# Kernel optimization log

Measured on AMD Instinct MI355X. Metric: run time of the kernel, lower is better.

The kernel has to match this reference:

```python
import jax, jax.numpy as jnp
import numpy as np

B, S, D, H, O = 256, 512, 256, 256, 128  # batch==hidden per the module's zeros(H,H) init


def setup_inputs() -> dict:
    key = jax.random.key(0)
    ks = jax.random.split(key, 20)
    sc = 0.05
    inp = {
        "x": jax.random.normal(ks[0], (B, S, D), jnp.float32),
        "Wgx_w": jax.random.normal(ks[1], (H, D), jnp.float32) * sc,
        "Wgx_b": jax.random.normal(ks[2], (H,), jnp.float32) * sc,
        "Wgh_w": jax.random.normal(ks[3], (H, H), jnp.float32) * sc,
        "Wgh_b": jax.random.normal(ks[4], (H,), jnp.float32) * sc,
        "Wix_w": jax.random.normal(ks[5], (H, D), jnp.float32) * sc,
        "Wix_b": jax.random.normal(ks[6], (H,), jnp.float32) * sc,
        "Wih_w": jax.random.normal(ks[7], (H, H), jnp.float32) * sc,
        "Wih_b": jax.random.normal(ks[8], (H,), jnp.float32) * sc,
        "Wfx_w": jax.random.normal(ks[9], (H, D), jnp.float32) * sc,
        "Wfx_b": jax.random.normal(ks[10], (H,), jnp.float32) * sc,
        "Wfh_w": jax.random.normal(ks[11], (H, H), jnp.float32) * sc,
        "Wfh_b": jax.random.normal(ks[12], (H,), jnp.float32) * sc,
        "Wox_w": jax.random.normal(ks[13], (H, D), jnp.float32) * sc,
        "Wox_b": jax.random.normal(ks[14], (H,), jnp.float32) * sc,
        "Woh_w": jax.random.normal(ks[15], (H, H), jnp.float32) * sc,
        "Woh_b": jax.random.normal(ks[16], (H,), jnp.float32) * sc,
        "Wph_w": jax.random.normal(ks[17], (O, H), jnp.float32) * sc,
        "Wph_b": jax.random.normal(ks[18], (O,), jnp.float32) * sc,
        "bg": jnp.zeros((B, H), jnp.float32),
        "bi": jnp.zeros((B, H), jnp.float32),
        "bf": jnp.zeros((B, H), jnp.float32),
        "bo": jnp.zeros((B, H), jnp.float32),
        "bp": jnp.zeros((B, O), jnp.float32),
    }
    return inp


def _lstm_forward(x, Wgx_w, Wgx_b, Wgh_w, Wgh_b, Wix_w, Wix_b, Wih_w, Wih_b,
                  Wfx_w, Wfx_b, Wfh_w, Wfh_b, Wox_w, Wox_b, Woh_w, Woh_b,
                  Wph_w, Wph_b, bg, bi, bf, bo, bp):
    b, s, d = x.shape
    h0 = jnp.zeros((b, Wgh_w.shape[0]), x.dtype)  # zeros(H,H) in source; B==H
    c0 = jnp.zeros_like(h0)
    # Precompute the input-to-gate projections for all timesteps (batched GEMM).
    xg = jnp.einsum('bsd,hd->sbh', x, Wgx_w) + Wgx_b + bg  # [S,B,H]
    xi = jnp.einsum('bsd,hd->sbh', x, Wix_w) + Wix_b + bi
    xf = jnp.einsum('bsd,hd->sbh', x, Wfx_w) + Wfx_b + bf
    xo = jnp.einsum('bsd,hd->sbh', x, Wox_w) + Wox_b + bo

    def step(carry, xs):
        h, c = carry
        xg_t, xi_t, xf_t, xo_t = xs
        g = jnp.tanh(xg_t + h @ Wgh_w.T + Wgh_b)
        i = jax.nn.sigmoid(xi_t + h @ Wih_w.T + Wih_b)
        f = jax.nn.sigmoid(xf_t + h @ Wfh_w.T + Wfh_b)
        o = jax.nn.sigmoid(xo_t + h @ Woh_w.T + Woh_b)
        c = g * i + c * f
        h = jnp.tanh(c) * o
        return (h, c), None

    (h, _), _ = jax.lax.scan(step, (h0, c0), (xg, xi, xf, xo))
    p = h @ Wph_w.T + Wph_b + bp
    return jax.nn.softmax(p, axis=1)


def reference(x, Wgx_w, Wgx_b, Wgh_w, Wgh_b, Wix_w, Wix_b, Wih_w, Wih_b,
              Wfx_w, Wfx_b, Wfh_w, Wfh_b, Wox_w, Wox_b, Woh_w, Woh_b,
              Wph_w, Wph_b, bg, bi, bf, bo, bp):
    return _lstm_forward(x, Wgx_w, Wgx_b, Wgh_w, Wgh_b, Wix_w, Wix_b, Wih_w, Wih_b,
                         Wfx_w, Wfx_b, Wfh_w, Wfh_b, Wox_w, Wox_b, Woh_w, Woh_b,
                         Wph_w, Wph_b, bg, bi, bf, bo, bp)
```

## Files before the change

kernel.cpp:

```cpp
#include <hip/hip_runtime.h>
#include <hip/hip_bf16.h>
#include <stdint.h>


typedef unsigned short u16;
typedef unsigned int   u32;
typedef __bf16  bf16x8 __attribute__((ext_vector_type(8)));
typedef float   f32x4  __attribute__((ext_vector_type(4)));

union U4 { uint4 u; bf16x8 b; u16 s[8]; };
union U2 { uint2 u; u16 s[4]; };

static __device__ __forceinline__ u16 f2b(float f){
  union { __hip_bfloat16 h; u16 u; } cv; cv.h = __float2bfloat16(f); return cv.u;
}
static __device__ __forceinline__ float b2f(u16 v){
  union { __hip_bfloat16 h; u16 u; } cv; cv.u = v; return __bfloat162float(cv.h);
}
static __device__ __forceinline__ float fsig(float x){
  return __builtin_amdgcn_rcpf(1.0f + __expf(-x));
}
static __device__ __forceinline__ float ftanh(float x){
  float ax = fabsf(x);
  float t  = __expf(-2.0f*ax);
  float r  = (1.0f - t) * __builtin_amdgcn_rcpf(1.0f + t);
  return copysignf(r, x);
}

struct PrepArgs {
  const float* wx[4]; const float* wh[4];
  const float* wxb[4]; const float* whb[4];
};

__global__ void k_prep(PrepArgs P, u16* __restrict__ WxP, u16* __restrict__ WhP,
                       float* __restrict__ biasj)
{
  int sIdx = blockIdx.x*256 + threadIdx.x;
  int lane = sIdx & 63, kb = (sIdx>>6)&7, jb = sIdx>>9;
  int jp = jb*16 + (lane & 15);
  int gate = jp & 3, hc = jp >> 2;
  int kbase = kb*32 + ((lane>>4)<<3);
  const float* wx = P.wx[gate];
  const float* wh = P.wh[gate];
  U4 ox, oh;
  #pragma unroll
  for (int e=0; e<8; e++){
    ox.s[e] = f2b(wx[hc*256 + kbase + e]);
    oh.s[e] = f2b(wh[hc*256 + kbase + e]);
  }
  *(uint4*)(WxP + (size_t)sIdx*8) = ox.u;
  *(uint4*)(WhP + (size_t)sIdx*8) = oh.u;
  if (sIdx < 1024){
    int g2 = sIdx & 3, h2 = sIdx >> 2;
    biasj[sIdx] = P.wxb[g2][h2] + P.whb[g2][h2];
  }
}

__global__ void k_convx(const float* __restrict__ x, u16* __restrict__ xbf)
{
  int tid = blockIdx.x*256 + threadIdx.x;
  int ch = tid & 31;
  int b  = (tid>>5) & 255;
  int s  = tid >> 13;
  const float* src = x + ((size_t)b*512 + s)*256 + ch*8;
  float4 f0 = *(const float4*)(src);
  float4 f1 = *(const float4*)(src + 4);
  U4 o;
  o.s[0]=f2b(f0.x); o.s[1]=f2b(f0.y); o.s[2]=f2b(f0.z); o.s[3]=f2b(f0.w);
  o.s[4]=f2b(f1.x); o.s[5]=f2b(f1.y); o.s[6]=f2b(f1.z); o.s[7]=f2b(f1.w);
  u32 byteoff = (u32)(s*256 + b)*512u + (((u32)ch*16u) ^ ((u32)(b&7)<<4));
  *(uint4*)((char*)xbf + byteoff) = o.u;
}

__launch_bounds__(512)
__global__ void k_gemm_x(const u16* __restrict__ xbf, const u16* __restrict__ WxP,
                         const float* __restrict__ biasj,
                         const float* __restrict__ bgg, const float* __restrict__ bii,
                         const float* __restrict__ bff, const float* __restrict__ boo,
                         u16* __restrict__ xcat)
{
  __shared__ u16 smA[128*256];
  int tid = threadIdx.x;
  int bid = blockIdx.x;
  int mt = bid >> 2, jt = bid & 3;
  int s = mt >> 1, b0 = (mt & 1)*128;

  const uint4* srcA = (const uint4*)(xbf + (size_t)(s*256 + b0)*256);
  uint4* dstA = (uint4*)smA;
  #pragma unroll
  for (int i=0; i<8; i++) dstA[tid + i*512] = srcA[tid + i*512];
  __syncthreads();

  int lane = tid & 63, wid = tid >> 6;
  int wm = wid >> 2, wn = wid & 3;
  int r16 = lane & 15, khi = lane >> 4;

  f32x4 acc[4][4] = {};
  #pragma unroll
  for (int kb=0; kb<8; kb++){
    bf16x8 a[4];
    #pragma unroll
    for (int mb=0; mb<4; mb++){
      int row = wm*64 + mb*16 + r16;
      u32 abyte = (u32)row*512u + ((u32)((kb*32 + khi*8)*2) ^ ((u32)(row&7)<<4));
      U4 t; t.u = *(const uint4*)((const char*)smA + abyte);
      a[mb] = t.b;
    }
    #pragma unroll
    for (int nb=0; nb<4; nb++){
      int jbg = jt*16 + wn*4 + nb;
      U4 t; t.u = *(const uint4*)(WxP + (size_t)((jbg*8 + kb)*64 + lane)*8);
      #pragma unroll
      for (int mb=0; mb<4; mb++)
        acc[mb][nb] = __builtin_amdgcn_mfma_f32_16x16x32_bf16(a[mb], t.b, acc[mb][nb], 0,0,0);
    }
  }

  int gate = r16 & 3;
  const float* bb = (gate==0) ? bgg : (gate==1) ? bii : (gate==2) ? bff : boo;
  #pragma unroll
  for (int nb=0; nb<4; nb++){
    int jp = jt*256 + wn*64 + nb*16 + r16;
    int hc = jp >> 2;
    float bj = biasj[jp];
    int w_l = wn*2 + (nb>>1);
    int sub = nb & 1;
    #pragma unroll
    for (int mb=0; mb<4; mb++){
      int grp = (b0>>4) + wm*4 + mb;
      U2 pk;
      #pragma unroll
      for (int r=0; r<4; r++){
        int b = b0 + wm*64 + mb*16 + khi*4 + r;
        pk.s[r] = f2b(acc[mb][nb][r] + bj + bb[b*256 + hc]);
      }
      size_t idx = (((size_t)s*16 + grp)*4 + jt)*4096
                 + (size_t)(w_l*64 + khi*16 + r16)*8 + sub*4;
      *(uint2*)(xcat + idx) = pk.u;
    }
  }
}

__launch_bounds__(512, 2)
__global__ void k_lstm(const u16* __restrict__ xcat2, const u16* __restrict__ WhP,
                       u16* __restrict__ hx, int* __restrict__ cnt,
                       float* __restrict__ hfin)
{
  __shared__ u16 hA[2][4096];
  int tid = threadIdx.x, lane = tid & 63, w = tid >> 6;
  int bid = blockIdx.x;
  int xcd = bid & 7, slot = bid >> 3;
  int grp = xcd*2 + (slot>>2), cb = slot & 3;
  int r16 = lane & 15, khi = lane >> 4;
  int gate = r16 & 3, hcl = r16 >> 2;

  bf16x8 wreg[2][8];
  #pragma unroll
  for (int nb=0; nb<2; nb++){
    int jb16 = cb*16 + w*2 + nb;
    #pragma unroll
    for (int kb=0; kb<8; kb++){
      U4 t; t.u = *(const uint4*)(WhP + (size_t)((jb16*8 + kb)*64 + lane)*8);
      wreg[nb][kb] = t.b;
    }
  }

  for (int i=tid; i<4096; i+=512) hA[0][i] = 0;
  __syncthreads();

  const u16* xbase = xcat2 + ((size_t)grp*4 + cb)*4096 + (size_t)tid*8;
  U4 xr; xr.u = *(const uint4*)(xbase);

  float c[2][4] = {};

  for (int t=0; t<512; t++){
    int par = t & 1;
    int tn = (t < 511) ? t+1 : 511;
    U4 xn; xn.u = *(const uint4*)(xbase + (size_t)tn*262144);

    f32x4 acc[2] = {};
    #pragma unroll
    for (int kb=0; kb<8; kb++){
      u32 ab = (u32)r16*512u + (((u32)(kb*64 + khi*16)) ^ ((u32)(r16&7)<<4));
      U4 ta; ta.u = *(const uint4*)((const char*)hA[par] + ab);
      acc[0] = __builtin_amdgcn_mfma_f32_16x16x32_bf16(ta.b, wreg[0][kb], acc[0], 0,0,0);
      acc[1] = __builtin_amdgcn_mfma_f32_16x16x32_bf16(ta.b, wreg[1][kb], acc[1], 0,0,0);
    }

    u16* hxN = hx + (size_t)(((t+1)&1)*16 + grp)*4096;

    #pragma unroll
    for (int nb=0; nb<2; nb++){
      int hc = cb*64 + w*8 + nb*4 + hcl;
      #pragma unroll
      for (int r=0; r<4; r++){
        float v = acc[nb][r] + b2f(xr.s[nb*4+r]);
        float a = (gate==0) ? ftanh(v) : fsig(v);
        float gi = a * __shfl_xor(a, 1);
        float fv = __shfl_xor(a, 2);
        float ov = __shfl_xor(a, 3);
        float cn = gi + c[nb][r]*fv;
        c[nb][r] = cn;
        float hv = ftanh(cn)*ov;
        if (gate == 0){
          u16 hb16 = f2b(hv);
          int b = khi*4 + r;
          hxN[b*256 + hc] = hb16;
          *(u16*)((char*)hA[par^1] +
                  ((u32)b*512u + (((u32)hc*2u) ^ ((u32)(b&7)<<4)))) = hb16;
          if (t == 511) hfin[(grp*16 + b)*256 + hc] = hv;
        }
      }
    }

    __syncthreads();
    if (tid == 0){
      int* cc = cnt + grp*2 + ((t+1)&1);
      __hip_atomic_fetch_add(cc, 1, __ATOMIC_RELEASE, __HIP_MEMORY_SCOPE_AGENT);
      int tgt = 4*((t>>1) + 1);
      while (__hip_atomic_load(cc, __ATOMIC_ACQUIRE, __HIP_MEMORY_SCOPE_AGENT) < tgt)
        __builtin_amdgcn_s_sleep(1);
    }
    __syncthreads();
    if (tid < 384){
      int oc = tid >> 7, rem = tid & 127;
      int b = rem >> 3, hc8 = rem & 7;
      int cbo = (cb + 1 + oc) & 3;
      int hc = cbo*64 + hc8*8;
      U4 tv; tv.u = *(const uint4*)(hxN + b*256 + hc);
      *(uint4*)((char*)hA[par^1] +
                ((u32)b*512u + (((u32)hc*2u) ^ ((u32)(b&7)<<4)))) = tv.u;
    }
    __syncthreads();
    xr = xn;
  }
}

__global__ void k_proj(const float* __restrict__ hfin, const float* __restrict__ Wph_w,
                       const float* __restrict__ Wph_b, const float* __restrict__ bp,
                       float* __restrict__ out)
{
  __shared__ float hrow[256];
  __shared__ float pbuf[128];
  int b = blockIdx.x, tid = threadIdx.x;
  hrow[tid]       = hfin[b*256 + tid];
  hrow[tid + 128] = hfin[b*256 + 128 + tid];
  __syncthreads();
  const float* wr = Wph_w + (size_t)tid*256;
  float acc = Wph_b[tid] + bp[b*128 + tid];
  #pragma unroll 8
  for (int k=0; k<256; k++) acc += hrow[k]*wr[k];
  pbuf[tid] = acc;
  __syncthreads();
  float mx = -1e30f;
  for (int i=0; i<128; i++) mx = fmaxf(mx, pbuf[i]);
  float e = __expf(acc - mx);
  __syncthreads();
  pbuf[tid] = e;
  __syncthreads();
  float sum = 0.f;
  for (int i=0; i<128; i++) sum += pbuf[i];
  out[b*128 + tid] = e / sum;
}

extern "C" void kernel_launch(void* const* d_in, const int* in_sizes, int n_in,
                              void* d_out, int out_size, void* d_ws, size_t ws_size,
                              hipStream_t stream)
{
  (void)in_sizes; (void)n_in; (void)out_size; (void)ws_size;
  const float* x     = (const float*)d_in[0];
  const float* Wph_w = (const float*)d_in[17];
  const float* Wph_b = (const float*)d_in[18];
  const float* bg    = (const float*)d_in[19];
  const float* bi    = (const float*)d_in[20];
  const float* bf    = (const float*)d_in[21];
  const float* bo    = (const float*)d_in[22];
  const float* bp    = (const float*)d_in[23];

  PrepArgs P;
  for (int g=0; g<4; g++){
    P.wx[g]  = (const float*)d_in[1 + 4*g];
    P.wxb[g] = (const float*)d_in[2 + 4*g];
    P.wh[g]  = (const float*)d_in[3 + 4*g];
    P.whb[g] = (const float*)d_in[4 + 4*g];
  }

  char* ws = (char*)d_ws;
  u16*   xcat  = (u16*)(ws);
  u16*   xbf   = (u16*)(ws + 268435456);
  u16*   hx    = (u16*)(ws + 268435456);
  int*   cnt   = (int*)(ws + 268435456 + 262144);
  u16*   WxP   = (u16*)(ws + 268435456 + 67108864);
  u16*   WhP   = (u16*)(ws + 268435456 + 67108864 + 524288);
  float* biasj = (float*)(ws + 268435456 + 67108864 + 1048576);
  float* hfin  = (float*)(ws + 268435456 + 67108864 + 1048576 + 4096);

  k_prep <<<128,   256, 0, stream>>>(P, WxP, WhP, biasj);
  k_convx<<<16384, 256, 0, stream>>>(x, xbf);
  k_gemm_x<<<4096, 512, 0, stream>>>(xbf, WxP, biasj, bg, bi, bf, bo, xcat);
  hipMemsetAsync(cnt, 0, 128, stream);
  k_lstm <<<64,    512, 0, stream>>>(xcat, WhP, hx, cnt, hfin);
  k_proj <<<256,   128, 0, stream>>>(hfin, Wph_w, Wph_b, bp, (float*)d_out);
}
```

Before: 2.389 ms.

## Split LSTM recurrence across two blocks per group with overlapped partial GEMM

Each batch group of the recurrent kernel is now handled by two blocks instead of four, each owning all four gates for 128 hidden units, so gate activations need no cross-lane shuffles. The weight layout and the x-projection output layout are reordered to match. Each block computes the partial recurrent product from its own freshly written hidden half before waiting for its peer. It replaces the shared counter barrier with a per-peer flag, so the local half of the next step's product overlaps the inter-block wait. The cost is twice the weight registers per thread and half as many blocks in flight.

```diff
diff --git a/kernel.cpp b/kernel.cpp
--- a/kernel.cpp
+++ b/kernel.cpp
@@ -9,7 +9,6 @@
 typedef float   f32x4  __attribute__((ext_vector_type(4)));
 
 union U4 { uint4 u; bf16x8 b; u16 s[8]; };
-union U2 { uint2 u; u16 s[4]; };
 
 static __device__ __forceinline__ u16 f2b(float f){
   union { __hip_bfloat16 h; u16 u; } cv; cv.h = __float2bfloat16(f); return cv.u;
@@ -37,8 +36,8 @@
 {
   int sIdx = blockIdx.x*256 + threadIdx.x;
   int lane = sIdx & 63, kb = (sIdx>>6)&7, jb = sIdx>>9;
-  int jp = jb*16 + (lane & 15);
-  int gate = jp & 3, hc = jp >> 2;
+  int hcl = lane & 15;
+  int gate = jb & 3, hc = ((jb>>2)<<4) | hcl;
   int kbase = kb*32 + ((lane>>4)<<3);
   const float* wx = P.wx[gate];
   const float* wh = P.wh[gate];
@@ -51,7 +50,7 @@
   *(uint4*)(WxP + (size_t)sIdx*8) = ox.u;
   *(uint4*)(WhP + (size_t)sIdx*8) = oh.u;
   if (sIdx < 1024){
-    int g2 = sIdx & 3, h2 = sIdx >> 2;
+    int g2 = (sIdx>>4)&3, h2 = ((sIdx>>6)<<4)|(sIdx&15);
     biasj[sIdx] = P.wxb[g2][h2] + P.whb[g2][h2];
   }
 }
@@ -116,48 +115,52 @@
     }
   }
 
-  int gate = r16 & 3;
-  const float* bb = (gate==0) ? bgg : (gate==1) ? bii : (gate==2) ? bff : boo;
-  #pragma unroll
-  for (int nb=0; nb<4; nb++){
-    int jp = jt*256 + wn*64 + nb*16 + r16;
-    int hc = jp >> 2;
-    float bj = biasj[jp];
-    int w_l = wn*2 + (nb>>1);
-    int sub = nb & 1;
-    #pragma unroll
-    for (int mb=0; mb<4; mb++){
-      int grp = (b0>>4) + wm*4 + mb;
-      U2 pk;
+  int hc  = (jt*4 + wn)*16 + r16;
+  int lw  = (jt&1)*4 + wn;
+  int cbv = jt >> 1;
+  int ltid = lw*64 + khi*16 + r16;
+  const float* btab[4] = {bgg, bii, bff, boo};
+  float bj[4];
+  #pragma unroll
+  for (int nb=0; nb<4; nb++) bj[nb] = biasj[jt*256 + wn*64 + nb*16 + r16];
+
+  #pragma unroll
+  for (int mb=0; mb<4; mb++){
+    int grp = (b0>>4) + wm*4 + mb;
+    U4 o1, o2;
+    #pragma unroll
+    for (int nb=0; nb<4; nb++){
       #pragma unroll
       for (int r=0; r<4; r++){
         int b = b0 + wm*64 + mb*16 + khi*4 + r;
-        pk.s[r] = f2b(acc[mb][nb][r] + bj + bb[b*256 + hc]);
+        float v = acc[mb][nb][r] + bj[nb] + btab[nb][b*256 + hc];
+        if (nb < 2) o1.s[nb*4 + r] = f2b(v);
+        else        o2.s[(nb-2)*4 + r] = f2b(v);
       }
-      size_t idx = (((size_t)s*16 + grp)*4 + jt)*4096
-                 + (size_t)(w_l*64 + khi*16 + r16)*8 + sub*4;
-      *(uint2*)(xcat + idx) = pk.u;
-    }
+    }
+    size_t base = (size_t)(s*32 + grp*2 + cbv)*8192 + (size_t)ltid*8;
+    *(uint4*)(xcat + base)        = o1.u;
+    *(uint4*)(xcat + base + 4096) = o2.u;
   }
 }
 
 __launch_bounds__(512, 2)
 __global__ void k_lstm(const u16* __restrict__ xcat2, const u16* __restrict__ WhP,
-                       u16* __restrict__ hx, int* __restrict__ cnt,
+                       u16* __restrict__ hx, int* __restrict__ flags,
                        float* __restrict__ hfin)
 {
   __shared__ u16 hA[2][4096];
   int tid = threadIdx.x, lane = tid & 63, w = tid >> 6;
   int bid = blockIdx.x;
-  int xcd = bid & 7, slot = bid >> 3;
-  int grp = xcd*2 + (slot>>2), cb = slot & 3;
+  int grp = (bid & 7)*2 + ((bid >> 3) & 1);
+  int cb  = bid >> 4;
   int r16 = lane & 15, khi = lane >> 4;
-  int gate = r16 & 3, hcl = r16 >> 2;
-
-  bf16x8 wreg[2][8];
-  #pragma unroll
-  for (int nb=0; nb<2; nb++){
-    int jb16 = cb*16 + w*2 + nb;
+  int hc  = cb*128 + w*16 + r16;
+
+  bf16x8 wreg[4][8];
+  #pragma unroll
+  for (int nb=0; nb<4; nb++){
+    int jb16 = cb*32 + w*4 + nb;
     #pragma unroll
     for (int kb=0; kb<8; kb++){
       U4 t; t.u = *(const uint4*)(WhP + (size_t)((jb16*8 + kb)*64 + lane)*8);
@@ -168,71 +171,112 @@
   for (int i=tid; i<4096; i+=512) hA[0][i] = 0;
   __syncthreads();
 
-  const u16* xbase = xcat2 + ((size_t)grp*4 + cb)*4096 + (size_t)tid*8;
-  U4 xr; xr.u = *(const uint4*)(xbase);
-
-  float c[2][4] = {};
-
-  for (int t=0; t<512; t++){
+  const u16* xbase = xcat2 + (size_t)(grp*2 + cb)*8192 + (size_t)tid*8;
+  U4 xa, xb;
+  xa.u = *(const uint4*)(xbase);
+  xb.u = *(const uint4*)(xbase + 4096);
+
+  float c[4] = {0.f,0.f,0.f,0.f};
+  f32x4 acc[4] = {};
+  int skb0 = (cb^1)*4, okb0 = cb*4;
+
+  for (int t=0; t<511; t++){
     int par = t & 1;
-    int tn = (t < 511) ? t+1 : 511;
-    U4 xn; xn.u = *(const uint4*)(xbase + (size_t)tn*262144);
-
-    f32x4 acc[2] = {};
-    #pragma unroll
-    for (int kb=0; kb<8; kb++){
+    U4 xa_n, xb_n;
+    {
+      const u16* xn = xbase + (size_t)(t+1)*262144;
+      xa_n.u = *(const uint4*)(xn);
+      xb_n.u = *(const uint4*)(xn + 4096);
+    }
+
+    #pragma unroll
+    for (int k=0; k<4; k++){
+      int kb = skb0 + k;
       u32 ab = (u32)r16*512u + (((u32)(kb*64 + khi*16)) ^ ((u32)(r16&7)<<4));
       U4 ta; ta.u = *(const uint4*)((const char*)hA[par] + ab);
-      acc[0] = __builtin_amdgcn_mfma_f32_16x16x32_bf16(ta.b, wreg[0][kb], acc[0], 0,0,0);
-      acc[1] = __builtin_amdgcn_mfma_f32_16x16x32_bf16(ta.b, wreg[1][kb], acc[1], 0,0,0);
-    }
-
-    u16* hxN = hx + (size_t)(((t+1)&1)*16 + grp)*4096;
-
-    #pragma unroll
-    for (int nb=0; nb<2; nb++){
-      int hc = cb*64 + w*8 + nb*4 + hcl;
-      #pragma unroll
-      for (int r=0; r<4; r++){
-        float v = acc[nb][r] + b2f(xr.s[nb*4+r]);
-        float a = (gate==0) ? ftanh(v) : fsig(v);
-        float gi = a * __shfl_xor(a, 1);
-        float fv = __shfl_xor(a, 2);
-        float ov = __shfl_xor(a, 3);
-        float cn = gi + c[nb][r]*fv;
-        c[nb][r] = cn;
-        float hv = ftanh(cn)*ov;
-        if (gate == 0){
-          u16 hb16 = f2b(hv);
-          int b = khi*4 + r;
-          hxN[b*256 + hc] = hb16;
-          *(u16*)((char*)hA[par^1] +
-                  ((u32)b*512u + (((u32)hc*2u) ^ ((u32)(b&7)<<4)))) = hb16;
-          if (t == 511) hfin[(grp*16 + b)*256 + hc] = hv;
-        }
-      }
+      #pragma unroll
+      for (int nb=0; nb<4; nb++)
+        acc[nb] = __builtin_amdgcn_mfma_f32_16x16x32_bf16(ta.b, wreg[nb][kb], acc[nb], 0,0,0);
+    }
+
+    int pn = (t+1) & 1;
+    u16* hxN = hx + (size_t)(pn*16 + grp)*4096;
+
+    #pragma unroll
+    for (int r=0; r<4; r++){
+      float gv = ftanh(acc[0][r] + b2f(xa.s[0+r]));
+      float iv = fsig (acc[1][r] + b2f(xa.s[4+r]));
+      float fv = fsig (acc[2][r] + b2f(xb.s[0+r]));
+      float ov = fsig (acc[3][r] + b2f(xb.s[4+r]));
+      float cn = gv*iv + c[r]*fv;
+      c[r] = cn;
+      float hv = ftanh(cn)*ov;
+      int b = khi*4 + r;
+      u16 hb16 = f2b(hv);
+      *(u16*)((char*)hA[par^1] +
+              ((u32)b*512u + (((u32)hc*2u) ^ ((u32)(b&7)<<4)))) = hb16;
+      hxN[b*256 + hc] = hb16;
     }
 
     __syncthreads();
+
+    int val = (t>>1) + 1;
+    if (tid == 0)
+      __hip_atomic_store(&flags[((grp*2 + pn)*2 + cb)*32], val,
+                         __ATOMIC_RELEASE, __HIP_MEMORY_SCOPE_AGENT);
+
+    #pragma unroll
+    for (int nb=0; nb<4; nb++) acc[nb] = (f32x4){0.f,0.f,0.f,0.f};
+    #pragma unroll
+    for (int k=0; k<4; k++){
+      int kb = okb0 + k;
+      u32 ab = (u32)r16*512u + (((u32)(kb*64 + khi*16)) ^ ((u32)(r16&7)<<4));
+      U4 ta; ta.u = *(const uint4*)((const char*)hA[par^1] + ab);
+      #pragma unroll
+      for (int nb=0; nb<4; nb++)
+        acc[nb] = __builtin_amdgcn_mfma_f32_16x16x32_bf16(ta.b, wreg[nb][kb], acc[nb], 0,0,0);
+    }
+
     if (tid == 0){
-      int* cc = cnt + grp*2 + ((t+1)&1);
-      __hip_atomic_fetch_add(cc, 1, __ATOMIC_RELEASE, __HIP_MEMORY_SCOPE_AGENT);
-      int tgt = 4*((t>>1) + 1);
-      while (__hip_atomic_load(cc, __ATOMIC_ACQUIRE, __HIP_MEMORY_SCOPE_AGENT) < tgt)
+      const int* sf = &flags[((grp*2 + pn)*2 + (cb^1))*32];
+      while (__hip_atomic_load(sf, __ATOMIC_ACQUIRE, __HIP_MEMORY_SCOPE_AGENT) < val)
         __builtin_amdgcn_s_sleep(1);
     }
     __syncthreads();
-    if (tid < 384){
-      int oc = tid >> 7, rem = tid & 127;
-      int b = rem >> 3, hc8 = rem & 7;
-      int cbo = (cb + 1 + oc) & 3;
-      int hc = cbo*64 + hc8*8;
-      U4 tv; tv.u = *(const uint4*)(hxN + b*256 + hc);
+
+    if (tid < 256){
+      int b = tid >> 4, hcc = (tid & 15)*8;
+      int hcs = (cb^1)*128 + hcc;
+      U4 tv; tv.u = *(const uint4*)(hxN + b*256 + hcs);
       *(uint4*)((char*)hA[par^1] +
-                ((u32)b*512u + (((u32)hc*2u) ^ ((u32)(b&7)<<4)))) = tv.u;
+                ((u32)b*512u + (((u32)(hcs*2)) ^ ((u32)(b&7)<<4)))) = tv.u;
     }
     __syncthreads();
-    xr = xn;
+    xa = xa_n; xb = xb_n;
+  }
+
+  {
+    int par = 1;
+    #pragma unroll
+    for (int k=0; k<4; k++){
+      int kb = skb0 + k;
+      u32 ab = (u32)r16*512u + (((u32)(kb*64 + khi*16)) ^ ((u32)(r16&7)<<4));
+      U4 ta; ta.u = *(const uint4*)((const char*)hA[par] + ab);
+      #pragma unroll
+      for (int nb=0; nb<4; nb++)
+        acc[nb] = __builtin_amdgcn_mfma_f32_16x16x32_bf16(ta.b, wreg[nb][kb], acc[nb], 0,0,0);
+    }
+    #pragma unroll
+    for (int r=0; r<4; r++){
+      float gv = ftanh(acc[0][r] + b2f(xa.s[0+r]));
+      float iv = fsig (acc[1][r] + b2f(xa.s[4+r]));
+      float fv = fsig (acc[2][r] + b2f(xb.s[0+r]));
+      float ov = fsig (acc[3][r] + b2f(xb.s[4+r]));
+      float cn = gv*iv + c[r]*fv;
+      float hv = ftanh(cn)*ov;
+      int b = khi*4 + r;
+      hfin[(grp*16 + b)*256 + hc] = hv;
+    }
   }
 }
 
@@ -289,7 +333,7 @@
   u16*   xcat  = (u16*)(ws);
   u16*   xbf   = (u16*)(ws + 268435456);
   u16*   hx    = (u16*)(ws + 268435456);
-  int*   cnt   = (int*)(ws + 268435456 + 262144);
+  int*   flags = (int*)(ws + 268435456 + 262144);
   u16*   WxP   = (u16*)(ws + 268435456 + 67108864);
   u16*   WhP   = (u16*)(ws + 268435456 + 67108864 + 524288);
   float* biasj = (float*)(ws + 268435456 + 67108864 + 1048576);
@@ -298,7 +342,7 @@
   k_prep <<<128,   256, 0, stream>>>(P, WxP, WhP, biasj);
   k_convx<<<16384, 256, 0, stream>>>(x, xbf);
   k_gemm_x<<<4096, 512, 0, stream>>>(xbf, WxP, biasj, bg, bi, bf, bo, xcat);
-  hipMemsetAsync(cnt, 0, 128, stream);
-  k_lstm <<<64,    512, 0, stream>>>(xcat, WhP, hx, cnt, hfin);
+  hipMemsetAsync(flags, 0, 8192, stream);
+  k_lstm <<<32,    512, 0, stream>>>(xcat, WhP, hx, flags, hfin);
   k_proj <<<256,   128, 0, stream>>>(hfin, Wph_w, Wph_b, bp, (float*)d_out);
 }
```

New measurement: 5.018 ms. 110% more time.
